# Optimization experiments

Measured on AMD Instinct MI355X. Metric: run time of the kernel, lower is better.

## Reference

```python
import jax, jax.numpy as jnp
import numpy as np

DIM = 1024
NUM_HEADS = 16
HEAD_DIM = DIM // NUM_HEADS


def setup_inputs() -> dict:
    key = jax.random.key(0)
    k1, k2, k3 = jax.random.split(key, 3)
    B, T = 2, 2048
    x = jax.random.normal(k1, (B, T, DIM), dtype=jnp.float32)
    # qkv: Linear(dim, 3*dim, bias=False); torch weight shape [3*dim, dim]
    w_qkv = jax.random.normal(k2, (3 * DIM, DIM), dtype=jnp.float32) * (1.0 / np.sqrt(DIM))
    # out_proj: Linear(dim, dim, bias=False) (zeros in orig init; random for a meaningful baseline)
    w_out = jax.random.normal(k3, (DIM, DIM), dtype=jnp.float32) * (1.0 / np.sqrt(DIM))
    return {"x": x, "w_qkv": w_qkv, "w_out": w_out}


def reference(x, w_qkv, w_out):
    B, T, C = x.shape
    H, D = NUM_HEADS, HEAD_DIM
    qkv = jnp.einsum("btc,fc->btf", x, w_qkv)            # [B,T,3C]
    qkv = qkv.reshape(B, T, 3, H, D).transpose(2, 0, 3, 1, 4)  # [3,B,H,T,D]
    q, k, v = qkv[0], qkv[1], qkv[2]
    scale = 1.0 / np.sqrt(D)
    scores = jnp.einsum("bhtd,bhsd->bhts", q, k) * scale  # [B,H,T,T]
    causal = jnp.tril(jnp.ones((T, T), dtype=bool))
    scores = jnp.where(causal, scores, -jnp.inf)
    attn = jax.nn.softmax(scores, axis=-1)
    out = jnp.einsum("bhts,bhsd->bhtd", attn, v)          # [B,H,T,D]
    out = out.transpose(0, 2, 1, 3).reshape(B, T, C)       # [B,T,C]
    return jnp.einsum("btc,oc->bto", out, w_out)
```

## Files before the change

kernel.cpp:

```cpp
#include <hip/hip_runtime.h>
#include <hip/hip_bf16.h>

typedef __attribute__((ext_vector_type(8))) short vbf8;
typedef __attribute__((ext_vector_type(4))) float vf4;
typedef __attribute__((ext_vector_type(4))) unsigned int vu4;

#define MFMA16(a, b, c) __builtin_amdgcn_mfma_f32_16x16x32_bf16((a), (b), (c), 0, 0, 0)

__device__ __forceinline__ unsigned short f2bf(float f) {
    unsigned int u = __float_as_uint(f);
    u += 0x7fffu + ((u >> 16) & 1u);
    return (unsigned short)(u >> 16);
}

__device__ __forceinline__ unsigned int cvtpk(float a, float b) {
    unsigned int r;
    asm("v_cvt_pk_bf16_f32 %0, %1, %2" : "=v"(r) : "v"(a), "v"(b));
    return r;
}

__device__ __forceinline__ void gload_lds16(const void* g, void* l) {
    __builtin_amdgcn_global_load_lds(
        (const __attribute__((address_space(1))) unsigned int*)(unsigned long long)g,
        (__attribute__((address_space(3))) unsigned int*)(unsigned long long)l,
        16, 0, 0);
}

__global__ __launch_bounds__(256) void cvt_all(
    const float* __restrict__ x, const float* __restrict__ wq, const float* __restrict__ wo,
    unsigned short* __restrict__ xb, unsigned short* __restrict__ wqb, unsigned short* __restrict__ wob)
{
    int i = blockIdx.x * 256 + threadIdx.x;
    const float* src;
    unsigned short* dst;
    int off;
    if (i < 1048576)      { src = x;  dst = xb;  off = i; }
    else if (i < 1835008) { src = wq; dst = wqb; off = i - 1048576; }
    else                  { src = wo; dst = wob; off = i - 1835008; }
    float4 v = ((const float4*)src)[off];
    ushort4 o;
    o.x = f2bf(v.x); o.y = f2bf(v.y); o.z = f2bf(v.z); o.w = f2bf(v.w);
    ((ushort4*)dst)[off] = o;
}

template <int EPI>
__global__ __launch_bounds__(256) void gemm_bt(
    const unsigned short* __restrict__ A, const unsigned short* __restrict__ Bt,
    int M, int N, int K,
    float* __restrict__ Cf,
    unsigned short* __restrict__ Qo, unsigned short* __restrict__ Ko, unsigned short* __restrict__ Vo)
{
    __shared__ __align__(16) unsigned short sA[128 * 64];
    __shared__ __align__(16) unsigned short sB[128 * 64];

    const int tid = threadIdx.x;
    const int lane = tid & 63;
    const int w = tid >> 6;
    const int wr = w >> 1, wc = w & 1;
    const int l16 = lane & 15, lhi = lane >> 4;
    const int bm = blockIdx.y, bn = blockIdx.x;
    const int row0 = bm * 128, col0 = bn * 128;

    vf4 acc[4][4] = {};

    for (int k0 = 0; k0 < K; k0 += 64) {
#pragma unroll
        for (int i = 0; i < 4; ++i) {
            int p = i * 256 + tid;
            int r = p >> 3, cb = p & 7;
            int cs = cb ^ (r & 7);
            gload_lds16(A + (size_t)(row0 + r) * K + k0 + (cs << 3), &sA[p << 3]);
            gload_lds16(Bt + (size_t)(col0 + r) * K + k0 + (cs << 3), &sB[p << 3]);
        }
        __syncthreads();
#pragma unroll
        for (int kk = 0; kk < 2; ++kk) {
            const int cb = kk * 4 + lhi;
            vbf8 af[4], bfr[4];
#pragma unroll
            for (int mt = 0; mt < 4; ++mt) {
                int r = wr * 64 + mt * 16 + l16;
                af[mt] = *(const vbf8*)&sA[(r << 6) + ((cb ^ (r & 7)) << 3)];
            }
#pragma unroll
            for (int nt = 0; nt < 4; ++nt) {
                int r = wc * 64 + nt * 16 + l16;
                bfr[nt] = *(const vbf8*)&sB[(r << 6) + ((cb ^ (r & 7)) << 3)];
            }
#pragma unroll
            for (int mt = 0; mt < 4; ++mt)
#pragma unroll
                for (int nt = 0; nt < 4; ++nt)
                    acc[mt][nt] = MFMA16(af[mt], bfr[nt], acc[mt][nt]);
        }
        __syncthreads();
    }

#pragma unroll
    for (int mt = 0; mt < 4; ++mt) {
#pragma unroll
        for (int nt = 0; nt < 4; ++nt) {
#pragma unroll
            for (int r = 0; r < 4; ++r) {
                int row = row0 + wr * 64 + mt * 16 + lhi * 4 + r;
                int col = col0 + wc * 64 + nt * 16 + l16;
                float v = acc[mt][nt][r];
                if (EPI == 0) {
                    Cf[(size_t)row * N + col] = v;
                } else {
                    int which = col >> 10, rem = col & 1023;
                    int h = rem >> 6, d = rem & 63;
                    int b = row >> 11, t = row & 2047;
                    size_t bh = (size_t)(b * 16 + h);
                    if (which == 0)      Qo[(bh * 2048 + t) * 64 + d] = f2bf(v * 0.18033688011112042f);
                    else if (which == 1) Ko[(bh * 2048 + t) * 64 + d] = f2bf(v);
                    else                 Vo[(bh * 64 + d) * 2048 + t] = f2bf(v);
                }
            }
        }
    }
}

__global__ __launch_bounds__(512, 4) void attn_fwd4(
    const unsigned short* __restrict__ Q, const unsigned short* __restrict__ Kp,
    const unsigned short* __restrict__ Vt, unsigned short* __restrict__ att)
{
    __shared__ __align__(16) unsigned short sK[2][128 * 64];
    __shared__ __align__(16) unsigned short sV[2][64 * 128];

    const int tid = threadIdx.x;
    const int lane = tid & 63;
    const int w = tid >> 6;
    const int l16 = lane & 15, lhi = lane >> 4;
    const int bh = blockIdx.x & 31;
    const int j = blockIdx.x >> 5;
    const int band = (j < 8) ? (15 - j) : (j - 8);
    const size_t hoff = (size_t)bh * 2048 * 64;
    const unsigned short* Qh = Q + hoff;
    const unsigned short* Kh = Kp + hoff;
    const unsigned short* Vh = Vt + hoff;
    const int q0 = band * 128;
    const int qg = q0 + w * 16 + l16;
    const int ktLast = band;

    const int pA = tid, pB = 512 + tid;
    const int rKA = pA >> 3, cKA = pA & 7;
    const int rKB = pB >> 3, cKB = pB & 7;
    const int rVA = pA >> 4, cVA = pA & 15;
    const int rVB = pB >> 4, cVB = pB & 15;
    const unsigned short* pKA = Kh + (size_t)rKA * 64 + ((cKA ^ (rKA & 7)) << 3);
    const unsigned short* pKB = Kh + (size_t)rKB * 64 + ((cKB ^ (rKB & 7)) << 3);
    const unsigned short* pVA = Vh + (size_t)rVA * 2048 + ((cVA ^ (rVA & 7)) << 3);
    const unsigned short* pVB = Vh + (size_t)rVB * 2048 + ((cVB ^ (rVB & 7)) << 3);
    const int dA = pA << 3, dB = pB << 3;

    auto STAGE = [&](int buf, int k0) {
        gload_lds16(pKA + (size_t)k0 * 64, &sK[buf][dA]);
        gload_lds16(pKB + (size_t)k0 * 64, &sK[buf][dB]);
        gload_lds16(pVA + k0, &sV[buf][dA]);
        gload_lds16(pVB + k0, &sV[buf][dB]);
    };

    STAGE(0, 0);

    vbf8 qf[2];
#pragma unroll
    for (int kk = 0; kk < 2; ++kk)
        qf[kk] = *(const vbf8*)&Qh[(size_t)qg * 64 + kk * 32 + lhi * 8];

    vf4 oacc[4] = {};
    float m = -1e30f, lsum = 0.f;

    for (int kt = 0; kt <= ktLast; ++kt) {
        const int cur = kt & 1;
        const int k0 = kt * 128;
        if (kt < ktLast) {
            STAGE(cur ^ 1, k0 + 128);
            asm volatile("s_waitcnt vmcnt(4)" ::: "memory");
        } else {
            asm volatile("s_waitcnt vmcnt(0)" ::: "memory");
        }
        __builtin_amdgcn_s_barrier();
        __builtin_amdgcn_sched_barrier(0);

        const unsigned short* sKc = &sK[cur][0];
        const unsigned short* sVc = &sV[cur][0];

        vf4 sc[8] = {};
#pragma unroll
        for (int kk = 0; kk < 2; ++kk) {
#pragma unroll
            for (int nt = 0; nt < 8; ++nt) {
                int rr = nt * 16 + l16;
                vbf8 kf = *(const vbf8*)&sKc[(rr << 6) + ((((kk << 2) + lhi) ^ (rr & 7)) << 3)];
                sc[nt] = MFMA16(kf, qf[kk], sc[nt]);
            }
        }

        if (kt == ktLast) {
#pragma unroll
            for (int nt = 0; nt < 8; ++nt)
#pragma unroll
                for (int r = 0; r < 4; ++r) {
                    int kg = k0 + nt * 16 + lhi * 4 + r;
                    if (kg > qg) sc[nt][r] = -1e30f;
                }
        }

        float m4[8];
#pragma unroll
        for (int nt = 0; nt < 8; ++nt)
            m4[nt] = fmaxf(fmaxf(sc[nt][0], sc[nt][1]), fmaxf(sc[nt][2], sc[nt][3]));
        float pm = fmaxf(fmaxf(fmaxf(m4[0], m4[1]), fmaxf(m4[2], m4[3])),
                         fmaxf(fmaxf(m4[4], m4[5]), fmaxf(m4[6], m4[7])));
        pm = fmaxf(pm, __shfl_xor(pm, 16, 64));
        pm = fmaxf(pm, __shfl_xor(pm, 32, 64));

        if (!__all(pm - m <= 8.0f)) {
            float mn = fmaxf(m, pm);
            float alpha = exp2f(m - mn);
            lsum *= alpha;
#pragma unroll
            for (int dt = 0; dt < 4; ++dt)
#pragma unroll
                for (int r = 0; r < 4; ++r) oacc[dt][r] *= alpha;
            m = mn;
        }

        float rs4[8];
#pragma unroll
        for (int nt = 0; nt < 8; ++nt) {
#pragma unroll
            for (int r = 0; r < 4; ++r) sc[nt][r] = exp2f(sc[nt][r] - m);
            rs4[nt] = (sc[nt][0] + sc[nt][1]) + (sc[nt][2] + sc[nt][3]);
        }
        float rs = ((rs4[0] + rs4[1]) + (rs4[2] + rs4[3])) +
                   ((rs4[4] + rs4[5]) + (rs4[6] + rs4[7]));
        rs += __shfl_xor(rs, 16, 64);
        rs += __shfl_xor(rs, 32, 64);
        lsum += rs;

        unsigned int pk0[8], pk1[8];
#pragma unroll
        for (int nt = 0; nt < 8; ++nt) {
            pk0[nt] = cvtpk(sc[nt][0], sc[nt][1]);
            pk1[nt] = cvtpk(sc[nt][2], sc[nt][3]);
        }

        const int srcA = l16 + ((lhi & 1) ? 32 : 0);
        const int srcB = srcA + 16;
        const bool hiSel = (lhi >> 1) != 0;
#pragma unroll
        for (int kk = 0; kk < 4; ++kk) {
            unsigned int a0e = __shfl((int)pk0[2 * kk], srcA, 64);
            unsigned int a1e = __shfl((int)pk1[2 * kk], srcA, 64);
            unsigned int b0e = __shfl((int)pk0[2 * kk], srcB, 64);
            unsigned int b1e = __shfl((int)pk1[2 * kk], srcB, 64);
            unsigned int a0o = __shfl((int)pk0[2 * kk + 1], srcA, 64);
            unsigned int a1o = __shfl((int)pk1[2 * kk + 1], srcA, 64);
            unsigned int b0o = __shfl((int)pk0[2 * kk + 1], srcB, 64);
            unsigned int b1o = __shfl((int)pk1[2 * kk + 1], srcB, 64);
            vu4 uw;
            uw.x = hiSel ? a0o : a0e;
            uw.y = hiSel ? a1o : a1e;
            uw.z = hiSel ? b0o : b0e;
            uw.w = hiSel ? b1o : b1e;
            vbf8 pf = __builtin_bit_cast(vbf8, uw);
#pragma unroll
            for (int dt = 0; dt < 4; ++dt) {
                int rr = dt * 16 + l16;
                vbf8 vfr = *(const vbf8*)&sVc[(rr << 7) + ((((kk << 2) + lhi) ^ (rr & 7)) << 3)];
                oacc[dt] = MFMA16(vfr, pf, oacc[dt]);
            }
        }
        __builtin_amdgcn_s_barrier();
        __builtin_amdgcn_sched_barrier(0);
    }

    const float inv = 1.0f / lsum;
    unsigned short* so = &sK[0][0] + w * 1024;
#pragma unroll
    for (int dt = 0; dt < 4; ++dt)
#pragma unroll
        for (int r = 0; r < 4; ++r)
            so[l16 * 64 + (((dt * 2 + (lhi >> 1)) ^ (l16 & 7)) << 3) + (lhi & 1) * 4 + r] =
                f2bf(oacc[dt][r] * inv);
    __syncthreads();

    const int b = bh >> 4, h = bh & 15;
    const int qr = lane >> 2;
    const int cj = lane & 3;
    vbf8 o1 = *(const vbf8*)&so[qr * 64 + (((cj * 2 + 0) ^ (qr & 7)) << 3)];
    vbf8 o2 = *(const vbf8*)&so[qr * 64 + (((cj * 2 + 1) ^ (qr & 7)) << 3)];
    const int qrow = q0 + w * 16 + qr;
    unsigned short* dst = att + ((size_t)(b * 2048 + qrow)) * 1024 + h * 64 + cj * 16;
    *(vbf8*)dst = o1;
    *(vbf8*)(dst + 8) = o2;
}

extern "C" void kernel_launch(void* const* d_in, const int* in_sizes, int n_in,
                              void* d_out, int out_size, void* d_ws, size_t ws_size,
                              hipStream_t stream) {
    const float* x = (const float*)d_in[0];
    const float* w_qkv = (const float*)d_in[1];
    const float* w_out = (const float*)d_in[2];
    float* out = (float*)d_out;

    char* ws = (char*)d_ws;
    unsigned short* xb   = (unsigned short*)(ws);
    unsigned short* wqb  = (unsigned short*)(ws + (8ull << 20));
    unsigned short* wob  = (unsigned short*)(ws + (14ull << 20));
    unsigned short* Qb   = (unsigned short*)(ws + (16ull << 20));
    unsigned short* Kb   = (unsigned short*)(ws + (24ull << 20));
    unsigned short* Vb   = (unsigned short*)(ws + (32ull << 20));
    unsigned short* attb = (unsigned short*)(ws + (40ull << 20));

    cvt_all<<<8192, 256, 0, stream>>>(x, w_qkv, w_out, xb, wqb, wob);

    gemm_bt<1><<<dim3(3072 / 128, 4096 / 128), 256, 0, stream>>>(
        xb, wqb, 4096, 3072, 1024, nullptr, Qb, Kb, Vb);

    attn_fwd4<<<16 * 32, 512, 0, stream>>>(Qb, Kb, Vb, attb);

    gemm_bt<0><<<dim3(1024 / 128, 4096 / 128), 256, 0, stream>>>(
        attb, wob, 4096, 1024, 1024, out, nullptr, nullptr, nullptr);
}
```

Baseline: 118.4 us.

## Replace LDS-tiled attention with single-wave blocks loading K/V directly from global

Rewrites the attention kernel so each 64-thread block handles 32 query rows (two 16-row groups) and reads K and V fragments straight from global memory into registers, with no LDS staging, double buffering or block barriers. The grid grows from 512 to 2048 blocks to give finer-grained causal load balancing and more parallelism. The trade-off is that K/V reuse across waves now depends on L2/L1 caching instead of shared memory, and global load latency is no longer overlapped by an explicit prefetch pipeline.

```diff
diff --git a/kernel.cpp b/kernel.cpp
--- a/kernel.cpp
+++ b/kernel.cpp
@@ -121,145 +121,157 @@
     }
 }
 
-__global__ __launch_bounds__(512, 4) void attn_fwd4(
+__global__ __launch_bounds__(64, 2) void attn_direct(
     const unsigned short* __restrict__ Q, const unsigned short* __restrict__ Kp,
     const unsigned short* __restrict__ Vt, unsigned short* __restrict__ att)
 {
-    __shared__ __align__(16) unsigned short sK[2][128 * 64];
-    __shared__ __align__(16) unsigned short sV[2][64 * 128];
-
-    const int tid = threadIdx.x;
-    const int lane = tid & 63;
-    const int w = tid >> 6;
+    __shared__ __align__(16) unsigned short so[2][16 * 64];
+
+    const int lane = threadIdx.x;
     const int l16 = lane & 15, lhi = lane >> 4;
     const int bh = blockIdx.x & 31;
-    const int j = blockIdx.x >> 5;
-    const int band = (j < 8) ? (15 - j) : (j - 8);
+    const int qt = 63 - (blockIdx.x >> 5);
+    const int q0 = qt * 32;
     const size_t hoff = (size_t)bh * 2048 * 64;
     const unsigned short* Qh = Q + hoff;
     const unsigned short* Kh = Kp + hoff;
     const unsigned short* Vh = Vt + hoff;
-    const int q0 = band * 128;
-    const int qg = q0 + w * 16 + l16;
-    const int ktLast = band;
-
-    const int pA = tid, pB = 512 + tid;
-    const int rKA = pA >> 3, cKA = pA & 7;
-    const int rKB = pB >> 3, cKB = pB & 7;
-    const int rVA = pA >> 4, cVA = pA & 15;
-    const int rVB = pB >> 4, cVB = pB & 15;
-    const unsigned short* pKA = Kh + (size_t)rKA * 64 + ((cKA ^ (rKA & 7)) << 3);
-    const unsigned short* pKB = Kh + (size_t)rKB * 64 + ((cKB ^ (rKB & 7)) << 3);
-    const unsigned short* pVA = Vh + (size_t)rVA * 2048 + ((cVA ^ (rVA & 7)) << 3);
-    const unsigned short* pVB = Vh + (size_t)rVB * 2048 + ((cVB ^ (rVB & 7)) << 3);
-    const int dA = pA << 3, dB = pB << 3;
-
-    auto STAGE = [&](int buf, int k0) {
-        gload_lds16(pKA + (size_t)k0 * 64, &sK[buf][dA]);
-        gload_lds16(pKB + (size_t)k0 * 64, &sK[buf][dB]);
-        gload_lds16(pVA + k0, &sV[buf][dA]);
-        gload_lds16(pVB + k0, &sV[buf][dB]);
-    };
-
-    STAGE(0, 0);
-
-    vbf8 qf[2];
-#pragma unroll
-    for (int kk = 0; kk < 2; ++kk)
-        qf[kk] = *(const vbf8*)&Qh[(size_t)qg * 64 + kk * 32 + lhi * 8];
-
-    vf4 oacc[4] = {};
-    float m = -1e30f, lsum = 0.f;
+    const int qg0 = q0 + l16, qg1 = q0 + 16 + l16;
+    const int ktLast = qt >> 1;
+
+    vbf8 qf0[2], qf1[2];
+#pragma unroll
+    for (int kk = 0; kk < 2; ++kk) {
+        qf0[kk] = *(const vbf8*)&Qh[(size_t)qg0 * 64 + kk * 32 + lhi * 8];
+        qf1[kk] = *(const vbf8*)&Qh[(size_t)qg1 * 64 + kk * 32 + lhi * 8];
+    }
+
+    vf4 o0[4] = {}, o1[4] = {};
+    float m0 = -1e30f, m1 = -1e30f, ls0 = 0.f, ls1 = 0.f;
+
+    const int srcA = l16 + ((lhi & 1) ? 32 : 0);
+    const int srcB = srcA + 16;
+    const bool hiSel = (lhi >> 1) != 0;
 
     for (int kt = 0; kt <= ktLast; ++kt) {
-        const int cur = kt & 1;
-        const int k0 = kt * 128;
-        if (kt < ktLast) {
-            STAGE(cur ^ 1, k0 + 128);
-            asm volatile("s_waitcnt vmcnt(4)" ::: "memory");
-        } else {
-            asm volatile("s_waitcnt vmcnt(0)" ::: "memory");
-        }
-        __builtin_amdgcn_s_barrier();
-        __builtin_amdgcn_sched_barrier(0);
-
-        const unsigned short* sKc = &sK[cur][0];
-        const unsigned short* sVc = &sV[cur][0];
-
-        vf4 sc[8] = {};
-#pragma unroll
-        for (int kk = 0; kk < 2; ++kk) {
-#pragma unroll
-            for (int nt = 0; nt < 8; ++nt) {
-                int rr = nt * 16 + l16;
-                vbf8 kf = *(const vbf8*)&sKc[(rr << 6) + ((((kk << 2) + lhi) ^ (rr & 7)) << 3)];
-                sc[nt] = MFMA16(kf, qf[kk], sc[nt]);
-            }
-        }
+        const int k0 = kt * 64;
+
+        vbf8 kf[2][4];
+#pragma unroll
+        for (int kk = 0; kk < 2; ++kk)
+#pragma unroll
+            for (int nt = 0; nt < 4; ++nt)
+                kf[kk][nt] = *(const vbf8*)&Kh[(size_t)(k0 + nt * 16 + l16) * 64 + kk * 32 + lhi * 8];
+
+        vbf8 vf[2][4];
+#pragma unroll
+        for (int kk = 0; kk < 2; ++kk)
+#pragma unroll
+            for (int dt = 0; dt < 4; ++dt)
+                vf[kk][dt] = *(const vbf8*)&Vh[(size_t)(dt * 16 + l16) * 2048 + k0 + kk * 32 + lhi * 8];
+
+        vf4 sc0[4] = {}, sc1[4] = {};
+#pragma unroll
+        for (int kk = 0; kk < 2; ++kk)
+#pragma unroll
+            for (int nt = 0; nt < 4; ++nt) {
+                sc0[nt] = MFMA16(kf[kk][nt], qf0[kk], sc0[nt]);
+                sc1[nt] = MFMA16(kf[kk][nt], qf1[kk], sc1[nt]);
+            }
 
         if (kt == ktLast) {
 #pragma unroll
-            for (int nt = 0; nt < 8; ++nt)
+            for (int nt = 0; nt < 4; ++nt)
 #pragma unroll
                 for (int r = 0; r < 4; ++r) {
                     int kg = k0 + nt * 16 + lhi * 4 + r;
-                    if (kg > qg) sc[nt][r] = -1e30f;
+                    if (kg > qg0) sc0[nt][r] = -1e30f;
+                    if (kg > qg1) sc1[nt][r] = -1e30f;
                 }
         }
 
-        float m4[8];
-#pragma unroll
-        for (int nt = 0; nt < 8; ++nt)
-            m4[nt] = fmaxf(fmaxf(sc[nt][0], sc[nt][1]), fmaxf(sc[nt][2], sc[nt][3]));
-        float pm = fmaxf(fmaxf(fmaxf(m4[0], m4[1]), fmaxf(m4[2], m4[3])),
-                         fmaxf(fmaxf(m4[4], m4[5]), fmaxf(m4[6], m4[7])));
-        pm = fmaxf(pm, __shfl_xor(pm, 16, 64));
-        pm = fmaxf(pm, __shfl_xor(pm, 32, 64));
-
-        if (!__all(pm - m <= 8.0f)) {
-            float mn = fmaxf(m, pm);
-            float alpha = exp2f(m - mn);
-            lsum *= alpha;
-#pragma unroll
-            for (int dt = 0; dt < 4; ++dt)
-#pragma unroll
-                for (int r = 0; r < 4; ++r) oacc[dt][r] *= alpha;
-            m = mn;
-        }
-
-        float rs4[8];
-#pragma unroll
-        for (int nt = 0; nt < 8; ++nt) {
-#pragma unroll
-            for (int r = 0; r < 4; ++r) sc[nt][r] = exp2f(sc[nt][r] - m);
-            rs4[nt] = (sc[nt][0] + sc[nt][1]) + (sc[nt][2] + sc[nt][3]);
-        }
-        float rs = ((rs4[0] + rs4[1]) + (rs4[2] + rs4[3])) +
-                   ((rs4[4] + rs4[5]) + (rs4[6] + rs4[7]));
-        rs += __shfl_xor(rs, 16, 64);
-        rs += __shfl_xor(rs, 32, 64);
-        lsum += rs;
-
-        unsigned int pk0[8], pk1[8];
-#pragma unroll
-        for (int nt = 0; nt < 8; ++nt) {
-            pk0[nt] = cvtpk(sc[nt][0], sc[nt][1]);
-            pk1[nt] = cvtpk(sc[nt][2], sc[nt][3]);
-        }
-
-        const int srcA = l16 + ((lhi & 1) ? 32 : 0);
-        const int srcB = srcA + 16;
-        const bool hiSel = (lhi >> 1) != 0;
-#pragma unroll
-        for (int kk = 0; kk < 4; ++kk) {
-            unsigned int a0e = __shfl((int)pk0[2 * kk], srcA, 64);
-            unsigned int a1e = __shfl((int)pk1[2 * kk], srcA, 64);
-            unsigned int b0e = __shfl((int)pk0[2 * kk], srcB, 64);
-            unsigned int b1e = __shfl((int)pk1[2 * kk], srcB, 64);
-            unsigned int a0o = __shfl((int)pk0[2 * kk + 1], srcA, 64);
-            unsigned int a1o = __shfl((int)pk1[2 * kk + 1], srcA, 64);
-            unsigned int b0o = __shfl((int)pk0[2 * kk + 1], srcB, 64);
-            unsigned int b1o = __shfl((int)pk1[2 * kk + 1], srcB, 64);
+        unsigned int pk0a[4], pk1a[4], pk0b[4], pk1b[4];
+        {
+            float m4[4];
+#pragma unroll
+            for (int nt = 0; nt < 4; ++nt)
+                m4[nt] = fmaxf(fmaxf(sc0[nt][0], sc0[nt][1]), fmaxf(sc0[nt][2], sc0[nt][3]));
+            float pm = fmaxf(fmaxf(m4[0], m4[1]), fmaxf(m4[2], m4[3]));
+            pm = fmaxf(pm, __shfl_xor(pm, 16, 64));
+            pm = fmaxf(pm, __shfl_xor(pm, 32, 64));
+            if (!__all(pm - m0 <= 8.0f)) {
+                float mn = fmaxf(m0, pm);
+                float a = exp2f(m0 - mn);
+                ls0 *= a;
+#pragma unroll
+                for (int dt = 0; dt < 4; ++dt)
+#pragma unroll
+                    for (int r = 0; r < 4; ++r) o0[dt][r] *= a;
+                m0 = mn;
+            }
+            float rs4[4];
+#pragma unroll
+            for (int nt = 0; nt < 4; ++nt) {
+#pragma unroll
+                for (int r = 0; r < 4; ++r) sc0[nt][r] = exp2f(sc0[nt][r] - m0);
+                rs4[nt] = (sc0[nt][0] + sc0[nt][1]) + (sc0[nt][2] + sc0[nt][3]);
+            }
+            float rs = (rs4[0] + rs4[1]) + (rs4[2] + rs4[3]);
+            rs += __shfl_xor(rs, 16, 64);
+            rs += __shfl_xor(rs, 32, 64);
+            ls0 += rs;
+#pragma unroll
+            for (int nt = 0; nt < 4; ++nt) {
+                pk0a[nt] = cvtpk(sc0[nt][0], sc0[nt][1]);
+                pk1a[nt] = cvtpk(sc0[nt][2], sc0[nt][3]);
+            }
+        }
+        {
+            float m4[4];
+#pragma unroll
+            for (int nt = 0; nt < 4; ++nt)
+                m4[nt] = fmaxf(fmaxf(sc1[nt][0], sc1[nt][1]), fmaxf(sc1[nt][2], sc1[nt][3]));
+            float pm = fmaxf(fmaxf(m4[0], m4[1]), fmaxf(m4[2], m4[3]));
+            pm = fmaxf(pm, __shfl_xor(pm, 16, 64));
+            pm = fmaxf(pm, __shfl_xor(pm, 32, 64));
+            if (!__all(pm - m1 <= 8.0f)) {
+                float mn = fmaxf(m1, pm);
+                float a = exp2f(m1 - mn);
+                ls1 *= a;
+#pragma unroll
+                for (int dt = 0; dt < 4; ++dt)
+#pragma unroll
+                    for (int r = 0; r < 4; ++r) o1[dt][r] *= a;
+                m1 = mn;
+            }
+            float rs4[4];
+#pragma unroll
+            for (int nt = 0; nt < 4; ++nt) {
+#pragma unroll
+                for (int r = 0; r < 4; ++r) sc1[nt][r] = exp2f(sc1[nt][r] - m1);
+                rs4[nt] = (sc1[nt][0] + sc1[nt][1]) + (sc1[nt][2] + sc1[nt][3]);
+            }
+            float rs = (rs4[0] + rs4[1]) + (rs4[2] + rs4[3]);
+            rs += __shfl_xor(rs, 16, 64);
+            rs += __shfl_xor(rs, 32, 64);
+            ls1 += rs;
+#pragma unroll
+            for (int nt = 0; nt < 4; ++nt) {
+                pk0b[nt] = cvtpk(sc1[nt][0], sc1[nt][1]);
+                pk1b[nt] = cvtpk(sc1[nt][2], sc1[nt][3]);
+            }
+        }
+
+#pragma unroll
+        for (int kk = 0; kk < 2; ++kk) {
+            unsigned int a0e = __shfl((int)pk0a[2 * kk], srcA, 64);
+            unsigned int a1e = __shfl((int)pk1a[2 * kk], srcA, 64);
+            unsigned int b0e = __shfl((int)pk0a[2 * kk], srcB, 64);
+            unsigned int b1e = __shfl((int)pk1a[2 * kk], srcB, 64);
+            unsigned int a0o = __shfl((int)pk0a[2 * kk + 1], srcA, 64);
+            unsigned int a1o = __shfl((int)pk1a[2 * kk + 1], srcA, 64);
+            unsigned int b0o = __shfl((int)pk0a[2 * kk + 1], srcB, 64);
+            unsigned int b1o = __shfl((int)pk1a[2 * kk + 1], srcB, 64);
             vu4 uw;
             uw.x = hiSel ? a0o : a0e;
             uw.y = hiSel ? a1o : a1e;
@@ -267,35 +279,54 @@
             uw.w = hiSel ? b1o : b1e;
             vbf8 pf = __builtin_bit_cast(vbf8, uw);
 #pragma unroll
-            for (int dt = 0; dt < 4; ++dt) {
-                int rr = dt * 16 + l16;
-                vbf8 vfr = *(const vbf8*)&sVc[(rr << 7) + ((((kk << 2) + lhi) ^ (rr & 7)) << 3)];
-                oacc[dt] = MFMA16(vfr, pf, oacc[dt]);
-            }
-        }
-        __builtin_amdgcn_s_barrier();
-        __builtin_amdgcn_sched_barrier(0);
-    }
-
-    const float inv = 1.0f / lsum;
-    unsigned short* so = &sK[0][0] + w * 1024;
+            for (int dt = 0; dt < 4; ++dt)
+                o0[dt] = MFMA16(vf[kk][dt], pf, o0[dt]);
+        }
+#pragma unroll
+        for (int kk = 0; kk < 2; ++kk) {
+            unsigned int a0e = __shfl((int)pk0b[2 * kk], srcA, 64);
+            unsigned int a1e = __shfl((int)pk1b[2 * kk], srcA, 64);
+            unsigned int b0e = __shfl((int)pk0b[2 * kk], srcB, 64);
+            unsigned int b1e = __shfl((int)pk1b[2 * kk], srcB, 64);
+            unsigned int a0o = __shfl((int)pk0b[2 * kk + 1], srcA, 64);
+            unsigned int a1o = __shfl((int)pk1b[2 * kk + 1], srcA, 64);
+            unsigned int b0o = __shfl((int)pk0b[2 * kk + 1], srcB, 64);
+            unsigned int b1o = __shfl((int)pk1b[2 * kk + 1], srcB, 64);
+            vu4 uw;
+            uw.x = hiSel ? a0o : a0e;
+            uw.y = hiSel ? a1o : a1e;
+            uw.z = hiSel ? b0o : b0e;
+            uw.w = hiSel ? b1o : b1e;
+            vbf8 pf = __builtin_bit_cast(vbf8, uw);
+#pragma unroll
+            for (int dt = 0; dt < 4; ++dt)
+                o1[dt] = MFMA16(vf[kk][dt], pf, o1[dt]);
+        }
+    }
+
+    const float inv0 = 1.0f / ls0, inv1 = 1.0f / ls1;
 #pragma unroll
     for (int dt = 0; dt < 4; ++dt)
 #pragma unroll
-        for (int r = 0; r < 4; ++r)
-            so[l16 * 64 + (((dt * 2 + (lhi >> 1)) ^ (l16 & 7)) << 3) + (lhi & 1) * 4 + r] =
-                f2bf(oacc[dt][r] * inv);
+        for (int r = 0; r < 4; ++r) {
+            int sw = (((dt * 2 + (lhi >> 1)) ^ (l16 & 7)) << 3) + (lhi & 1) * 4 + r;
+            so[0][l16 * 64 + sw] = f2bf(o0[dt][r] * inv0);
+            so[1][l16 * 64 + sw] = f2bf(o1[dt][r] * inv1);
+        }
     __syncthreads();
 
     const int b = bh >> 4, h = bh & 15;
     const int qr = lane >> 2;
     const int cj = lane & 3;
-    vbf8 o1 = *(const vbf8*)&so[qr * 64 + (((cj * 2 + 0) ^ (qr & 7)) << 3)];
-    vbf8 o2 = *(const vbf8*)&so[qr * 64 + (((cj * 2 + 1) ^ (qr & 7)) << 3)];
-    const int qrow = q0 + w * 16 + qr;
-    unsigned short* dst = att + ((size_t)(b * 2048 + qrow)) * 1024 + h * 64 + cj * 16;
-    *(vbf8*)dst = o1;
-    *(vbf8*)(dst + 8) = o2;
+#pragma unroll
+    for (int g = 0; g < 2; ++g) {
+        vbf8 t1 = *(const vbf8*)&so[g][qr * 64 + (((cj * 2 + 0) ^ (qr & 7)) << 3)];
+        vbf8 t2 = *(const vbf8*)&so[g][qr * 64 + (((cj * 2 + 1) ^ (qr & 7)) << 3)];
+        const int qrow = q0 + g * 16 + qr;
+        unsigned short* dst = att + ((size_t)(b * 2048 + qrow)) * 1024 + h * 64 + cj * 16;
+        *(vbf8*)dst = t1;
+        *(vbf8*)(dst + 8) = t2;
+    }
 }
 
 extern "C" void kernel_launch(void* const* d_in, const int* in_sizes, int n_in,
@@ -320,7 +351,7 @@
     gemm_bt<1><<<dim3(3072 / 128, 4096 / 128), 256, 0, stream>>>(
         xb, wqb, 4096, 3072, 1024, nullptr, Qb, Kb, Vb);
 
-    attn_fwd4<<<16 * 32, 512, 0, stream>>>(Qb, Kb, Vb, attb);
+    attn_direct<<<2048, 64, 0, stream>>>(Qb, Kb, Vb, attb);
 
     gemm_bt<0><<<dim3(1024 / 128, 4096 / 128), 256, 0, stream>>>(
         attb, wob, 4096, 1024, 1024, out, nullptr, nullptr, nullptr);
```

New measurement: 153.3 us. 29.5% more time.

## Shrink attention KV tile to 64, skip masked per-wave tiles, raise occupancy

Applied to the files above, without the earlier changes.

Cuts the attention K/V tile from 128 to 64 keys, which halves shared memory per block and lets occupancy rise to 6 blocks. Each wave now skips key tiles that lie entirely above its causal diagonal and applies the mask only where a tile crosses it, so less work is wasted on the diagonal. It also raises wave priority around the MFMA sections and orders blocks heaviest-band-first instead of interleaving bands. The cost is twice as many loop iterations, each with its own barriers and softmax reductions.

```diff
diff --git a/kernel.cpp b/kernel.cpp
--- a/kernel.cpp
+++ b/kernel.cpp
@@ -121,44 +121,35 @@
     }
 }
 
-__global__ __launch_bounds__(512, 4) void attn_fwd4(
+__global__ __launch_bounds__(512, 6) void attn_fwd5(
     const unsigned short* __restrict__ Q, const unsigned short* __restrict__ Kp,
     const unsigned short* __restrict__ Vt, unsigned short* __restrict__ att)
 {
-    __shared__ __align__(16) unsigned short sK[2][128 * 64];
-    __shared__ __align__(16) unsigned short sV[2][64 * 128];
+    __shared__ __align__(16) unsigned short sK[2][64 * 64];
+    __shared__ __align__(16) unsigned short sV[2][64 * 64];
 
     const int tid = threadIdx.x;
     const int lane = tid & 63;
     const int w = tid >> 6;
     const int l16 = lane & 15, lhi = lane >> 4;
     const int bh = blockIdx.x & 31;
-    const int j = blockIdx.x >> 5;
-    const int band = (j < 8) ? (15 - j) : (j - 8);
+    const int band = 15 - (blockIdx.x >> 5);
     const size_t hoff = (size_t)bh * 2048 * 64;
     const unsigned short* Qh = Q + hoff;
     const unsigned short* Kh = Kp + hoff;
     const unsigned short* Vh = Vt + hoff;
     const int q0 = band * 128;
     const int qg = q0 + w * 16 + l16;
-    const int ktLast = band;
-
-    const int pA = tid, pB = 512 + tid;
-    const int rKA = pA >> 3, cKA = pA & 7;
-    const int rKB = pB >> 3, cKB = pB & 7;
-    const int rVA = pA >> 4, cVA = pA & 15;
-    const int rVB = pB >> 4, cVB = pB & 15;
-    const unsigned short* pKA = Kh + (size_t)rKA * 64 + ((cKA ^ (rKA & 7)) << 3);
-    const unsigned short* pKB = Kh + (size_t)rKB * 64 + ((cKB ^ (rKB & 7)) << 3);
-    const unsigned short* pVA = Vh + (size_t)rVA * 2048 + ((cVA ^ (rVA & 7)) << 3);
-    const unsigned short* pVB = Vh + (size_t)rVB * 2048 + ((cVB ^ (rVB & 7)) << 3);
-    const int dA = pA << 3, dB = pB << 3;
+    const int ktLast = 2 * band + 1;
+
+    const int rK = tid >> 3, cK = tid & 7;
+    const unsigned short* pK = Kh + (size_t)rK * 64 + ((cK ^ (rK & 7)) << 3);
+    const unsigned short* pV = Vh + (size_t)rK * 2048 + ((cK ^ (rK & 7)) << 3);
+    const int dL = tid << 3;
 
     auto STAGE = [&](int buf, int k0) {
-        gload_lds16(pKA + (size_t)k0 * 64, &sK[buf][dA]);
-        gload_lds16(pKB + (size_t)k0 * 64, &sK[buf][dB]);
-        gload_lds16(pVA + k0, &sV[buf][dA]);
-        gload_lds16(pVB + k0, &sV[buf][dB]);
+        gload_lds16(pK + (size_t)k0 * 64, &sK[buf][dL]);
+        gload_lds16(pV + k0, &sV[buf][dL]);
     };
 
     STAGE(0, 0);
@@ -173,104 +164,108 @@
 
     for (int kt = 0; kt <= ktLast; ++kt) {
         const int cur = kt & 1;
-        const int k0 = kt * 128;
+        const int k0 = kt * 64;
         if (kt < ktLast) {
-            STAGE(cur ^ 1, k0 + 128);
-            asm volatile("s_waitcnt vmcnt(4)" ::: "memory");
+            STAGE(cur ^ 1, k0 + 64);
+            asm volatile("s_waitcnt vmcnt(2)" ::: "memory");
         } else {
             asm volatile("s_waitcnt vmcnt(0)" ::: "memory");
         }
         __builtin_amdgcn_s_barrier();
         __builtin_amdgcn_sched_barrier(0);
 
-        const unsigned short* sKc = &sK[cur][0];
-        const unsigned short* sVc = &sV[cur][0];
-
-        vf4 sc[8] = {};
-#pragma unroll
-        for (int kk = 0; kk < 2; ++kk) {
-#pragma unroll
-            for (int nt = 0; nt < 8; ++nt) {
-                int rr = nt * 16 + l16;
-                vbf8 kf = *(const vbf8*)&sKc[(rr << 6) + ((((kk << 2) + lhi) ^ (rr & 7)) << 3)];
-                sc[nt] = MFMA16(kf, qf[kk], sc[nt]);
-            }
-        }
-
-        if (kt == ktLast) {
-#pragma unroll
-            for (int nt = 0; nt < 8; ++nt)
-#pragma unroll
-                for (int r = 0; r < 4; ++r) {
-                    int kg = k0 + nt * 16 + lhi * 4 + r;
-                    if (kg > qg) sc[nt][r] = -1e30f;
+        if (k0 <= q0 + w * 16 + 15) {
+            const unsigned short* sKc = &sK[cur][0];
+            const unsigned short* sVc = &sV[cur][0];
+
+            vf4 sc[4] = {};
+            __builtin_amdgcn_s_setprio(1);
+#pragma unroll
+            for (int kk = 0; kk < 2; ++kk) {
+#pragma unroll
+                for (int nt = 0; nt < 4; ++nt) {
+                    int rr = nt * 16 + l16;
+                    vbf8 kf = *(const vbf8*)&sKc[(rr << 6) + ((((kk << 2) + lhi) ^ (rr & 7)) << 3)];
+                    sc[nt] = MFMA16(kf, qf[kk], sc[nt]);
                 }
-        }
-
-        float m4[8];
-#pragma unroll
-        for (int nt = 0; nt < 8; ++nt)
-            m4[nt] = fmaxf(fmaxf(sc[nt][0], sc[nt][1]), fmaxf(sc[nt][2], sc[nt][3]));
-        float pm = fmaxf(fmaxf(fmaxf(m4[0], m4[1]), fmaxf(m4[2], m4[3])),
-                         fmaxf(fmaxf(m4[4], m4[5]), fmaxf(m4[6], m4[7])));
-        pm = fmaxf(pm, __shfl_xor(pm, 16, 64));
-        pm = fmaxf(pm, __shfl_xor(pm, 32, 64));
-
-        if (!__all(pm - m <= 8.0f)) {
-            float mn = fmaxf(m, pm);
-            float alpha = exp2f(m - mn);
-            lsum *= alpha;
-#pragma unroll
-            for (int dt = 0; dt < 4; ++dt)
-#pragma unroll
-                for (int r = 0; r < 4; ++r) oacc[dt][r] *= alpha;
-            m = mn;
-        }
-
-        float rs4[8];
-#pragma unroll
-        for (int nt = 0; nt < 8; ++nt) {
-#pragma unroll
-            for (int r = 0; r < 4; ++r) sc[nt][r] = exp2f(sc[nt][r] - m);
-            rs4[nt] = (sc[nt][0] + sc[nt][1]) + (sc[nt][2] + sc[nt][3]);
-        }
-        float rs = ((rs4[0] + rs4[1]) + (rs4[2] + rs4[3])) +
-                   ((rs4[4] + rs4[5]) + (rs4[6] + rs4[7]));
-        rs += __shfl_xor(rs, 16, 64);
-        rs += __shfl_xor(rs, 32, 64);
-        lsum += rs;
-
-        unsigned int pk0[8], pk1[8];
-#pragma unroll
-        for (int nt = 0; nt < 8; ++nt) {
-            pk0[nt] = cvtpk(sc[nt][0], sc[nt][1]);
-            pk1[nt] = cvtpk(sc[nt][2], sc[nt][3]);
-        }
-
-        const int srcA = l16 + ((lhi & 1) ? 32 : 0);
-        const int srcB = srcA + 16;
-        const bool hiSel = (lhi >> 1) != 0;
-#pragma unroll
-        for (int kk = 0; kk < 4; ++kk) {
-            unsigned int a0e = __shfl((int)pk0[2 * kk], srcA, 64);
-            unsigned int a1e = __shfl((int)pk1[2 * kk], srcA, 64);
-            unsigned int b0e = __shfl((int)pk0[2 * kk], srcB, 64);
-            unsigned int b1e = __shfl((int)pk1[2 * kk], srcB, 64);
-            unsigned int a0o = __shfl((int)pk0[2 * kk + 1], srcA, 64);
-            unsigned int a1o = __shfl((int)pk1[2 * kk + 1], srcA, 64);
-            unsigned int b0o = __shfl((int)pk0[2 * kk + 1], srcB, 64);
-            unsigned int b1o = __shfl((int)pk1[2 * kk + 1], srcB, 64);
-            vu4 uw;
-            uw.x = hiSel ? a0o : a0e;
-            uw.y = hiSel ? a1o : a1e;
-            uw.z = hiSel ? b0o : b0e;
-            uw.w = hiSel ? b1o : b1e;
-            vbf8 pf = __builtin_bit_cast(vbf8, uw);
-#pragma unroll
-            for (int dt = 0; dt < 4; ++dt) {
-                int rr = dt * 16 + l16;
-                vbf8 vfr = *(const vbf8*)&sVc[(rr << 7) + ((((kk << 2) + lhi) ^ (rr & 7)) << 3)];
-                oacc[dt] = MFMA16(vfr, pf, oacc[dt]);
+            }
+            __builtin_amdgcn_s_setprio(0);
+
+            if (k0 + 63 > q0 + w * 16) {
+#pragma unroll
+                for (int nt = 0; nt < 4; ++nt)
+#pragma unroll
+                    for (int r = 0; r < 4; ++r) {
+                        int kg = k0 + nt * 16 + lhi * 4 + r;
+                        if (kg > qg) sc[nt][r] = -1e30f;
+                    }
+            }
+
+            float m4[4];
+#pragma unroll
+            for (int nt = 0; nt < 4; ++nt)
+                m4[nt] = fmaxf(fmaxf(sc[nt][0], sc[nt][1]), fmaxf(sc[nt][2], sc[nt][3]));
+            float pm = fmaxf(fmaxf(m4[0], m4[1]), fmaxf(m4[2], m4[3]));
+            pm = fmaxf(pm, __shfl_xor(pm, 16, 64));
+            pm = fmaxf(pm, __shfl_xor(pm, 32, 64));
+
+            if (!__all(pm - m <= 8.0f)) {
+                float mn = fmaxf(m, pm);
+                float alpha = exp2f(m - mn);
+                lsum *= alpha;
+#pragma unroll
+                for (int dt = 0; dt < 4; ++dt)
+#pragma unroll
+                    for (int r = 0; r < 4; ++r) oacc[dt][r] *= alpha;
+                m = mn;
+            }
+
+            float rs4[4];
+#pragma unroll
+            for (int nt = 0; nt < 4; ++nt) {
+#pragma unroll
+                for (int r = 0; r < 4; ++r) sc[nt][r] = exp2f(sc[nt][r] - m);
+                rs4[nt] = (sc[nt][0] + sc[nt][1]) + (sc[nt][2] + sc[nt][3]);
+            }
+            float rs = (rs4[0] + rs4[1]) + (rs4[2] + rs4[3]);
+            rs += __shfl_xor(rs, 16, 64);
+            rs += __shfl_xor(rs, 32, 64);
+            lsum += rs;
+
+            unsigned int pk0[4], pk1[4];
+#pragma unroll
+            for (int nt = 0; nt < 4; ++nt) {
+                pk0[nt] = cvtpk(sc[nt][0], sc[nt][1]);
+                pk1[nt] = cvtpk(sc[nt][2], sc[nt][3]);
+            }
+
+            const int srcA = l16 + ((lhi & 1) ? 32 : 0);
+            const int srcB = srcA + 16;
+            const bool hiSel = (lhi >> 1) != 0;
+#pragma unroll
+            for (int kk = 0; kk < 2; ++kk) {
+                unsigned int a0e = __shfl((int)pk0[2 * kk], srcA, 64);
+                unsigned int a1e = __shfl((int)pk1[2 * kk], srcA, 64);
+                unsigned int b0e = __shfl((int)pk0[2 * kk], srcB, 64);
+                unsigned int b1e = __shfl((int)pk1[2 * kk], srcB, 64);
+                unsigned int a0o = __shfl((int)pk0[2 * kk + 1], srcA, 64);
+                unsigned int a1o = __shfl((int)pk1[2 * kk + 1], srcA, 64);
+                unsigned int b0o = __shfl((int)pk0[2 * kk + 1], srcB, 64);
+                unsigned int b1o = __shfl((int)pk1[2 * kk + 1], srcB, 64);
+                vu4 uw;
+                uw.x = hiSel ? a0o : a0e;
+                uw.y = hiSel ? a1o : a1e;
+                uw.z = hiSel ? b0o : b0e;
+                uw.w = hiSel ? b1o : b1e;
+                vbf8 pf = __builtin_bit_cast(vbf8, uw);
+                __builtin_amdgcn_s_setprio(1);
+#pragma unroll
+                for (int dt = 0; dt < 4; ++dt) {
+                    int rr = dt * 16 + l16;
+                    vbf8 vfr = *(const vbf8*)&sVc[(rr << 6) + ((((kk << 2) + lhi) ^ (rr & 7)) << 3)];
+                    oacc[dt] = MFMA16(vfr, pf, oacc[dt]);
+                }
+                __builtin_amdgcn_s_setprio(0);
             }
         }
         __builtin_amdgcn_s_barrier();
@@ -320,7 +315,7 @@
     gemm_bt<1><<<dim3(3072 / 128, 4096 / 128), 256, 0, stream>>>(
         xb, wqb, 4096, 3072, 1024, nullptr, Qb, Kb, Vb);
 
-    attn_fwd4<<<16 * 32, 512, 0, stream>>>(Qb, Kb, Vb, attb);
+    attn_fwd5<<<16 * 32, 512, 0, stream>>>(Qb, Kb, Vb, attb);
 
     gemm_bt<0><<<dim3(1024 / 128, 4096 / 128), 256, 0, stream>>>(
         attb, wob, 4096, 1024, 1024, out, nullptr, nullptr, nullptr);
```

Result: slower. 129.9 us (+9.8%).
